# Optimization experiments

Hardware: AMD Instinct MI355X
Metric: run time of the kernel (lower is better)

Reference implementation:

```python
import jax, jax.numpy as jnp
import numpy as np

N_LAYER = 2
N_HEAD = 12
D = 768
B = 4
L = 1024
LN_EPS = 1e-6
NEG = jnp.float32(-1e9)


def setup_inputs() -> dict:
    key = jax.random.key(0)
    ks = jax.random.split(key, 12)
    s = 0.02
    wshp = (N_LAYER, 4, D, D)
    return {
        "h_a": jax.random.normal(ks[0], (B, L, D), jnp.float32),
        "h_b": jax.random.normal(ks[1], (B, L, D), jnp.float32),
        "adj_a": jax.random.randint(ks[2], (B, L, L), 0, 2, jnp.int32),
        "adj_b": jax.random.randint(ks[3], (B, L, L), 0, 2, jnp.int32),
        "adj_ab": jax.random.randint(ks[4], (B, L, L), 0, 2, jnp.int32),
        "adj_ba": jax.random.randint(ks[5], (B, L, L), 0, 2, jnp.int32),
        "Wq": jax.random.normal(ks[6], wshp, jnp.float32) * s,
        "Wk": jax.random.normal(ks[7], wshp, jnp.float32) * s,
        "Wv": jax.random.normal(ks[8], wshp, jnp.float32) * s,
        "Wf": jax.random.normal(ks[9], wshp, jnp.float32) * s,
        "ln_g": jnp.ones((N_LAYER, 4, D), jnp.float32),
        "ln_b": jnp.zeros((N_LAYER, 4, D), jnp.float32),
    }


def _mha(xq, xk, xv, mask, Wq, Wk, Wv, Wf, g, b):
    # xq: [B, Lq, D]; mask: [B, Lq, Lk] (0 = masked out)
    Bq, Lq, d = xq.shape
    dk = d // N_HEAD
    q = (xq @ Wq).reshape(Bq, Lq, N_HEAD, dk).transpose(0, 2, 1, 3)
    k = (xk @ Wk).reshape(Bq, -1, N_HEAD, dk).transpose(0, 2, 1, 3)
    v = (xv @ Wv).reshape(Bq, -1, N_HEAD, dk).transpose(0, 2, 1, 3)
    attn = jnp.einsum('bhqd,bhkd->bhqk', q, k) / jnp.sqrt(jnp.float32(dk))
    attn = jnp.where(mask[:, None, :, :] == 0, NEG, attn)
    attn = jax.nn.softmax(attn, axis=-1)
    o = jnp.einsum('bhqk,bhkd->bhqd', attn, v)
    o = o.transpose(0, 2, 1, 3).reshape(Bq, Lq, d)
    o = o @ Wf + xq  # residual (dropout is identity in eval)
    mu = jnp.mean(o, axis=-1, keepdims=True)
    var = jnp.var(o, axis=-1, keepdims=True)
    return (o - mu) * jax.lax.rsqrt(var + LN_EPS) * g + b


def reference(h_a, h_b, adj_a, adj_b, adj_ab, adj_ba, Wq, Wk, Wv, Wf, ln_g, ln_b):
    input_a, input_b = h_a, h_b
    for i in range(N_LAYER):
        a2a = _mha(h_a, h_a, h_a, adj_a, Wq[i, 0], Wk[i, 0], Wv[i, 0], Wf[i, 0], ln_g[i, 0], ln_b[i, 0])
        b2b = _mha(h_b, h_b, h_b, adj_b, Wq[i, 1], Wk[i, 1], Wv[i, 1], Wf[i, 1], ln_g[i, 1], ln_b[i, 1])
        a2b = _mha(h_b, h_a, h_a, adj_ab, Wq[i, 2], Wk[i, 2], Wv[i, 2], Wf[i, 2], ln_g[i, 2], ln_b[i, 2])
        b2a = _mha(h_a, h_b, h_b, adj_ba, Wq[i, 3], Wk[i, 3], Wv[i, 3], Wf[i, 3], ln_g[i, 3], ln_b[i, 3])
        h_a = jax.nn.relu(a2a + b2a)
        h_b = jax.nn.relu(b2b + a2b)
    return (input_a + h_a, input_b + h_b)
```

## Files before the change

### kernel.cpp

```cpp
#include <hip/hip_runtime.h>
#include <stdint.h>

#define NLAYER 2
#define NHEAD 12
#define D 768
#define BB 4
#define LL 1024
#define M (BB*LL)
#define DK 64

typedef unsigned short u16;
typedef unsigned int u32;
typedef unsigned long long u64;
typedef __attribute__((ext_vector_type(8))) __bf16 bf16x8;
typedef __attribute__((ext_vector_type(4))) float f32x4;

__device__ __forceinline__ u16 f2b(float f) {
  u32 u = __float_as_uint(f);
  u += 0x7fffu + ((u >> 16) & 1u);
  return (u16)(u >> 16);
}
__device__ __forceinline__ float b2f(u16 h) {
  return __uint_as_float(((u32)h) << 16);
}
__device__ __forceinline__ f32x4 mfma16(bf16x8 a, bf16x8 b, f32x4 c) {
  return __builtin_amdgcn_mfma_f32_16x16x32_bf16(a, b, c, 0, 0, 0);
}
__device__ __forceinline__ void gl_lds16(const u16* g, u16* l) {
  __builtin_amdgcn_global_load_lds((const __attribute__((address_space(1))) void*)(g),
                                   (__attribute__((address_space(3))) void*)(l), 16, 0, 0);
}

__global__ void cast_f32_bf16(const float* __restrict__ src, u16* __restrict__ dst, int n) {
  int i = (blockIdx.x * 256 + threadIdx.x) * 4;
  if (i + 3 < n) {
    float4 v = *(const float4*)(src + i);
    dst[i+0] = f2b(v.x); dst[i+1] = f2b(v.y); dst[i+2] = f2b(v.z); dst[i+3] = f2b(v.w);
  }
}

__global__ void wtrans(const float* __restrict__ Wq, const float* __restrict__ Wk,
                       const float* __restrict__ Wv, const float* __restrict__ Wf,
                       u16* __restrict__ wtr) {
  int z = blockIdx.z;
  int layer = z >> 4, mat = (z >> 2) & 3, s = z & 3;
  const float* src = (mat==0?Wq:mat==1?Wk:mat==2?Wv:Wf) + (size_t)(layer*4 + s)*D*D;
  u16* dst = wtr + (size_t)z*D*D;
  __shared__ float tile[32][33];
  int x0 = blockIdx.x*32, y0 = blockIdx.y*32;
  int tx = threadIdx.x & 31, ty = threadIdx.x >> 5;
  #pragma unroll
  for (int i=0;i<4;++i) tile[ty + i*8][tx] = src[(size_t)(y0 + ty + i*8)*D + x0 + tx];
  __syncthreads();
  #pragma unroll
  for (int i=0;i<4;++i) dst[(size_t)(x0 + ty + i*8)*D + y0 + tx] = f2b(tile[tx][ty + i*8]);
}

__global__ __launch_bounds__(256) void pack_adj(const int* __restrict__ a0, const int* __restrict__ a1,
                                                const int* __restrict__ a2, const int* __restrict__ a3,
                                                u64* __restrict__ mb) {
  const int s = blockIdx.y;
  const int* __restrict__ src = s==0?a0:s==1?a1:s==2?a2:a3;
  u64* dst = mb + (size_t)s * (BB*LL*LL/64);
  const int lane = threadIdx.x & 63;
  const int w0 = blockIdx.x*4 + (threadIdx.x>>6);
  const int wstep = gridDim.x*4;
  for (int w = w0; w < BB*LL*LL/64; w += wstep) {
    int v = src[(size_t)w*64 + lane];
    u64 m = __ballot(v != 0);
    if (lane == 0) dst[w] = m;
  }
}

__device__ __forceinline__ void gemm128(const u16* __restrict__ A, const u16* __restrict__ W,
                                        u16* __restrict__ C, int vtrans,
                                        int m0, int n0) {
  __shared__ __align__(16) u16 As[2][128*32];
  __shared__ __align__(16) u16 Bs[2][128*32];
  const int t = threadIdx.x;
  const int wave = t >> 6, lane = t & 63, lg = lane >> 4, lr = lane & 15;
  const int wr = wave >> 1, wc = wave & 1;
  f32x4 acc[4][4] = {};
  const int srow = wave*32 + (lane >> 2);
  const int scol = (lane & 3) << 3;
  const u16* ga0 = A + (size_t)(m0 + srow)*D + scol;
  const u16* gb0 = W + (size_t)(n0 + srow)*D + scol;
  const int l0 = (wave*32)*32, l1 = (wave*32 + 16)*32;

  for (int kk = 0; kk < D; kk += 64) {
    __syncthreads();
    #pragma unroll
    for (int hh=0; hh<2; ++hh) {
      const int ko = kk + hh*32;
      gl_lds16(ga0 + ko,        &As[hh][l0]);
      gl_lds16(ga0 + ko + 16*D, &As[hh][l1]);
      gl_lds16(gb0 + ko,        &Bs[hh][l0]);
      gl_lds16(gb0 + ko + 16*D, &Bs[hh][l1]);
    }
    __syncthreads();
    #pragma unroll
    for (int hh=0; hh<2; ++hh) {
      bf16x8 af[4], bfr[4];
      #pragma unroll
      for (int mi=0;mi<4;++mi) af[mi] = *(const bf16x8*)(&As[hh][(wr*64 + mi*16 + lr)*32 + lg*8]);
      #pragma unroll
      for (int ni=0;ni<4;++ni) bfr[ni] = *(const bf16x8*)(&Bs[hh][(wc*64 + ni*16 + lr)*32 + lg*8]);
      #pragma unroll
      for (int mi=0;mi<4;++mi)
        #pragma unroll
        for (int ni=0;ni<4;++ni)
          acc[mi][ni] = mfma16(af[mi], bfr[ni], acc[mi][ni]);
    }
  }

  if (!vtrans) {
    #pragma unroll
    for (int mi=0;mi<4;++mi)
      #pragma unroll
      for (int ni=0;ni<4;++ni) {
        int col = n0 + wc*64 + ni*16 + lr;
        #pragma unroll
        for (int r=0;r<4;++r) {
          int row = m0 + wr*64 + mi*16 + lg*4 + r;
          C[(size_t)row*D + col] = f2b(acc[mi][ni][r]);
        }
      }
  } else {
    #pragma unroll
    for (int mi=0;mi<4;++mi)
      #pragma unroll
      for (int ni=0;ni<4;++ni) {
        int col = n0 + wc*64 + ni*16 + lr;
        int h = col >> 6, d = col & 63;
        #pragma unroll
        for (int r=0;r<4;++r) {
          int row = m0 + wr*64 + mi*16 + lg*4 + r;
          int p = ((r >> 1) << 5) | (lg << 3) | (mi << 1) | (r & 1);
          int lperm = (row & ~63) | p;
          int b = row >> 10, l = lperm & 1023;
          C[(((size_t)((b*NHEAD + h)<<6) + d) << 10) + l] = f2b(acc[mi][ni][r]);
        }
      }
  }
}

__global__ __launch_bounds__(256) void qkv_gemm(const u16* __restrict__ hA, const u16* __restrict__ hB,
                        const u16* __restrict__ wtr,
                        u16* __restrict__ Qb, u16* __restrict__ Kb, u16* __restrict__ Vtb, int layer) {
  int bid = blockIdx.x + 32*(blockIdx.y + 6*blockIdx.z);
  int logical = (bid & 7)*288 + (bid >> 3);
  int z = logical / 192, rem = logical % 192;
  int x = rem / 6, y = rem % 6;
  int s = z / 3, which = z % 3;
  const u16* X;
  if (which == 0) X = (s==0||s==3) ? hA : hB;
  else            X = (s==0||s==2) ? hA : hB;
  const u16* W = wtr + (size_t)((layer*4 + which)*4 + s)*D*D;
  u16* Cb = (which==0 ? Qb : which==1 ? Kb : Vtb) + (size_t)s*M*D;
  gemm128(X, W, Cb, which == 2 ? 1 : 0, x*128, y*128);
}

__global__ __launch_bounds__(256) void oproj_gemm(const u16* __restrict__ Ob, const u16* __restrict__ wtr,
                          u16* __restrict__ OPb, int layer) {
  int bid = blockIdx.x + 32*(blockIdx.y + 6*blockIdx.z);
  int logical = (bid & 7)*96 + (bid >> 3);
  int s = logical / 192, rem = logical % 192;
  int x = rem / 6, y = rem % 6;
  const u16* W = wtr + (size_t)((layer*4 + 3)*4 + s)*D*D;
  gemm128(Ob + (size_t)s*M*D, W, OPb + (size_t)s*M*D, 0, x*128, y*128);
}

#define CSC 0.1803368801111204f

__global__ __launch_bounds__(512) void attn_kernel(const u16* __restrict__ Qb, const u16* __restrict__ Kb,
                           const u16* __restrict__ Vtb,
                           const u64* __restrict__ mbits,
                           u16* __restrict__ Ob) {
  int bid = blockIdx.x + 8*(blockIdx.y + 48*blockIdx.z);
  int logical = (bid & 7)*192 + (bid >> 3);
  const int qt = logical & 7;
  const int bhs = logical >> 3;
  const int s = bhs / 48;
  const int bh = bhs % 48;
  const int b = bh / NHEAD, h = bh % NHEAD;

  const int t = threadIdx.x, wave = t >> 6, lane = t & 63, lg = lane >> 4, lr = lane & 15;
  const u16* Q = Qb + (size_t)s*M*D;
  const u16* K = Kb + (size_t)s*M*D;
  u16* O = Ob + (size_t)s*M*D;
  const u64* mbs = mbits + (size_t)s*(BB*LL*LL/64) + (size_t)b*(LL*LL/64);

  __shared__ __align__(16) u16 Ks[64][72];
  __shared__ __align__(16) u16 Vts[64][72];

  const int q0 = qt*128 + wave*16;
  bf16x8 qf0 = *(const bf16x8*)(Q + (size_t)(b*LL + q0 + lr)*D + h*DK + lg*8);
  bf16x8 qf1 = *(const bf16x8*)(Q + (size_t)(b*LL + q0 + lr)*D + h*DK + 32 + lg*8);

  f32x4 of[4] = {};
  float lrow = 0.f;

  const int kr = t >> 3, kc = (t & 7) << 3;
  const u16* Kp  = K + (size_t)(b*LL + kr)*D + h*DK + kc;
  const u16* Vtp = Vtb + (size_t)s*M*D + ((size_t)(bh*64 + kr) << 10) + kc;

  uint4 ka = *(const uint4*)(Kp);
  uint4 va = *(const uint4*)(Vtp);
  const int mstride = LL/64;
  u64 mw = mbs[(size_t)(q0 + lr)*mstride];
  u64 mwn;

  for (int kt = 0; kt < LL; kt += 64) {
    __syncthreads();
    *(uint4*)(&Ks[kr][kc])  = ka;
    *(uint4*)(&Vts[kr][kc]) = va;
    if (kt + 64 < LL) {
      ka = *(const uint4*)(Kp + (size_t)(kt+64)*D);
      va = *(const uint4*)(Vtp + kt + 64);
      mwn = mbs[(size_t)(q0 + lr)*mstride + (kt >> 6) + 1];
    }
    __syncthreads();

    f32x4 sfr[4];
    __builtin_amdgcn_s_setprio(1);
    #pragma unroll
    for (int c=0;c<4;++c) {
      bf16x8 kf0 = *(const bf16x8*)(&Ks[c*16+lr][lg*8]);
      bf16x8 kf1 = *(const bf16x8*)(&Ks[c*16+lr][32 + lg*8]);
      f32x4 z = {0.f,0.f,0.f,0.f};
      z = mfma16(kf0, qf0, z);
      z = mfma16(kf1, qf1, z);
      sfr[c] = z;
    }
    __builtin_amdgcn_s_setprio(0);

    u32 wlo = (u32)(mw >> (lg*4));
    u32 whi = (u32)(mw >> (lg*4 + 32));
    float pw[4][4];
    #pragma unroll
    for (int c=0;c<4;++c) {
      u32 wsel = (c < 2) ? wlo : whi;
      int sh = (c & 1) << 4;
      #pragma unroll
      for (int r=0;r<4;++r) {
        float e = __builtin_amdgcn_exp2f(sfr[c][r]*CSC);
        e = ((wsel >> (sh + r)) & 1u) ? e : 0.f;
        pw[c][r] = e;
        lrow += e;
      }
    }
    mw = mwn;

    union { u32 u[4]; bf16x8 v; } a0, a1;
    #pragma unroll
    for (int c=0;c<4;++c) {
      a0.u[c] = (__float_as_uint(pw[c][0]) >> 16) | (__float_as_uint(pw[c][1]) & 0xffff0000u);
      a1.u[c] = (__float_as_uint(pw[c][2]) >> 16) | (__float_as_uint(pw[c][3]) & 0xffff0000u);
    }

    __builtin_amdgcn_s_setprio(1);
    #pragma unroll
    for (int ni=0;ni<4;++ni) {
      bf16x8 vf0 = *(const bf16x8*)(&Vts[ni*16+lr][lg*8]);
      bf16x8 vf1 = *(const bf16x8*)(&Vts[ni*16+lr][32 + lg*8]);
      of[ni] = mfma16(a0.v, vf0, of[ni]);
      of[ni] = mfma16(a1.v, vf1, of[ni]);
    }
    __builtin_amdgcn_s_setprio(0);
  }

  lrow += __shfl_xor(lrow, 16, 64);
  lrow += __shfl_xor(lrow, 32, 64);

  #pragma unroll
  for (int r=0;r<4;++r) {
    float l = __shfl(lrow, lg*4 + r, 64);
    float inv = 1.0f / fmaxf(l, 1e-35f);
    int row = b*LL + q0 + lg*4 + r;
    #pragma unroll
    for (int ni=0;ni<4;++ni)
      O[(size_t)row*D + h*DK + ni*16 + lr] = f2b(of[ni][r] * inv);
  }
}

__global__ __launch_bounds__(256) void epilogue(const u16* __restrict__ OPb,
                        u16* __restrict__ hA, u16* __restrict__ hB,
                        const float* __restrict__ lng, const float* __restrict__ lnb,
                        const float* __restrict__ inA, const float* __restrict__ inB,
                        float* __restrict__ outA, float* __restrict__ outB,
                        int layer, int last) {
  const int row = blockIdx.x;
  const int t = threadIdx.x;
  __shared__ float red[8];
  float lnv[4][3];
  #pragma unroll
  for (int s=0;s<4;++s) {
    const u16* xq = (s==0||s==3) ? hA : hB;
    float o[3]; float sum=0.f, sq=0.f;
    #pragma unroll
    for (int j=0;j<3;++j) {
      int c = t + j*256;
      float v = b2f(OPb[((size_t)s*M + row)*D + c]) + b2f(xq[(size_t)row*D + c]);
      o[j]=v; sum+=v; sq += v*v;
    }
    #pragma unroll
    for (int off=32; off>0; off>>=1) { sum += __shfl_down(sum, off, 64); sq += __shfl_down(sq, off, 64); }
    int wv = t>>6, ln = t&63;
    if (ln==0) { red[wv] = sum; red[4+wv] = sq; }
    __syncthreads();
    sum = red[0]+red[1]+red[2]+red[3];
    sq  = red[4]+red[5]+red[6]+red[7];
    __syncthreads();
    float mu = sum * (1.0f/D);
    float var = sq * (1.0f/D) - mu*mu;
    float rstd = rsqrtf(var + 1e-6f);
    #pragma unroll
    for (int j=0;j<3;++j) {
      int c = t + j*256;
      lnv[s][j] = (o[j]-mu)*rstd * lng[(layer*4+s)*D + c] + lnb[(layer*4+s)*D + c];
    }
  }
  #pragma unroll
  for (int j=0;j<3;++j) {
    int c = t + j*256;
    float ha = fmaxf(lnv[0][j]+lnv[3][j], 0.f);
    float hb = fmaxf(lnv[1][j]+lnv[2][j], 0.f);
    hA[(size_t)row*D + c] = f2b(ha);
    hB[(size_t)row*D + c] = f2b(hb);
    if (last) {
      outA[(size_t)row*D + c] = inA[(size_t)row*D + c] + ha;
      outB[(size_t)row*D + c] = inB[(size_t)row*D + c] + hb;
    }
  }
}

extern "C" void kernel_launch(void* const* d_in, const int* in_sizes, int n_in,
                              void* d_out, int out_size, void* d_ws, size_t ws_size,
                              hipStream_t stream) {
  const float* h_a = (const float*)d_in[0];
  const float* h_b = (const float*)d_in[1];
  const int* adjA  = (const int*)d_in[2];
  const int* adjB  = (const int*)d_in[3];
  const int* adjAB = (const int*)d_in[4];
  const int* adjBA = (const int*)d_in[5];
  const float* Wq  = (const float*)d_in[6];
  const float* Wk  = (const float*)d_in[7];
  const float* Wv  = (const float*)d_in[8];
  const float* Wf  = (const float*)d_in[9];
  const float* lng = (const float*)d_in[10];
  const float* lnb = (const float*)d_in[11];
  float* outA = (float*)d_out;
  float* outB = outA + (size_t)M*D;

  char* ws = (char*)d_ws;
  size_t off = 0;
  auto alloc = [&](size_t bytes) { void* p = ws + off; off += (bytes + 255) & ~(size_t)255; return p; };
  u16* wtr = (u16*)alloc((size_t)32*D*D*2);
  u16* hAb = (u16*)alloc((size_t)M*D*2);
  u16* hBb = (u16*)alloc((size_t)M*D*2);
  u16* Qb  = (u16*)alloc((size_t)4*M*D*2);
  u16* Kb  = (u16*)alloc((size_t)4*M*D*2);
  u16* Vtb = (u16*)alloc((size_t)4*M*D*2);
  u16* Ob  = (u16*)alloc((size_t)4*M*D*2);
  u64* mbits = (u64*)alloc((size_t)4*BB*LL*LL/64*8);
  u16* OPb = Qb;

  int n = M*D;
  cast_f32_bf16<<<dim3(n/4/256), 256, 0, stream>>>(h_a, hAb, n);
  cast_f32_bf16<<<dim3(n/4/256), 256, 0, stream>>>(h_b, hBb, n);
  wtrans<<<dim3(24,24,32), 256, 0, stream>>>(Wq, Wk, Wv, Wf, wtr);
  pack_adj<<<dim3(2048,4), 256, 0, stream>>>(adjA, adjB, adjAB, adjBA, mbits);

  for (int layer = 0; layer < NLAYER; ++layer) {
    qkv_gemm<<<dim3(32,6,12), 256, 0, stream>>>(hAb, hBb, wtr, Qb, Kb, Vtb, layer);
    attn_kernel<<<dim3(8,48,4), 512, 0, stream>>>(Qb, Kb, Vtb, mbits, Ob);
    oproj_gemm<<<dim3(32,6,4), 256, 0, stream>>>(Ob, wtr, OPb, layer);
    epilogue<<<dim3(M), 256, 0, stream>>>(OPb, hAb, hBb, lng, lnb, h_a, h_b, outA, outB,
                                          layer, layer == NLAYER-1 ? 1 : 0);
  }
}
```

Before: 482.8 us.

## Use 8 waves per GEMM tile and batch layernorm reductions in epilogue

```diff
diff --git a/kernel.cpp b/kernel.cpp
--- a/kernel.cpp
+++ b/kernel.cpp
@@ -79,36 +79,34 @@
   __shared__ __align__(16) u16 Bs[2][128*32];
   const int t = threadIdx.x;
   const int wave = t >> 6, lane = t & 63, lg = lane >> 4, lr = lane & 15;
-  const int wr = wave >> 1, wc = wave & 1;
-  f32x4 acc[4][4] = {};
-  const int srow = wave*32 + (lane >> 2);
+  const int wr = wave >> 2, wc = wave & 3;
+  f32x4 acc[4][2] = {};
+  const int srow = wave*16 + (lane >> 2);
   const int scol = (lane & 3) << 3;
   const u16* ga0 = A + (size_t)(m0 + srow)*D + scol;
   const u16* gb0 = W + (size_t)(n0 + srow)*D + scol;
-  const int l0 = (wave*32)*32, l1 = (wave*32 + 16)*32;
+  const int l0 = (wave*16)*32;
 
   for (int kk = 0; kk < D; kk += 64) {
     __syncthreads();
     #pragma unroll
     for (int hh=0; hh<2; ++hh) {
       const int ko = kk + hh*32;
-      gl_lds16(ga0 + ko,        &As[hh][l0]);
-      gl_lds16(ga0 + ko + 16*D, &As[hh][l1]);
-      gl_lds16(gb0 + ko,        &Bs[hh][l0]);
-      gl_lds16(gb0 + ko + 16*D, &Bs[hh][l1]);
+      gl_lds16(ga0 + ko, &As[hh][l0]);
+      gl_lds16(gb0 + ko, &Bs[hh][l0]);
     }
     __syncthreads();
     #pragma unroll
     for (int hh=0; hh<2; ++hh) {
-      bf16x8 af[4], bfr[4];
+      bf16x8 af[4], bfr[2];
       #pragma unroll
       for (int mi=0;mi<4;++mi) af[mi] = *(const bf16x8*)(&As[hh][(wr*64 + mi*16 + lr)*32 + lg*8]);
       #pragma unroll
-      for (int ni=0;ni<4;++ni) bfr[ni] = *(const bf16x8*)(&Bs[hh][(wc*64 + ni*16 + lr)*32 + lg*8]);
+      for (int ni=0;ni<2;++ni) bfr[ni] = *(const bf16x8*)(&Bs[hh][(wc*32 + ni*16 + lr)*32 + lg*8]);
       #pragma unroll
       for (int mi=0;mi<4;++mi)
         #pragma unroll
-        for (int ni=0;ni<4;++ni)
+        for (int ni=0;ni<2;++ni)
           acc[mi][ni] = mfma16(af[mi], bfr[ni], acc[mi][ni]);
     }
   }
@@ -117,8 +115,8 @@
     #pragma unroll
     for (int mi=0;mi<4;++mi)
       #pragma unroll
-      for (int ni=0;ni<4;++ni) {
-        int col = n0 + wc*64 + ni*16 + lr;
+      for (int ni=0;ni<2;++ni) {
+        int col = n0 + wc*32 + ni*16 + lr;
         #pragma unroll
         for (int r=0;r<4;++r) {
           int row = m0 + wr*64 + mi*16 + lg*4 + r;
@@ -129,8 +127,8 @@
     #pragma unroll
     for (int mi=0;mi<4;++mi)
       #pragma unroll
-      for (int ni=0;ni<4;++ni) {
-        int col = n0 + wc*64 + ni*16 + lr;
+      for (int ni=0;ni<2;++ni) {
+        int col = n0 + wc*32 + ni*16 + lr;
         int h = col >> 6, d = col & 63;
         #pragma unroll
         for (int r=0;r<4;++r) {
@@ -144,7 +142,7 @@
   }
 }
 
-__global__ __launch_bounds__(256) void qkv_gemm(const u16* __restrict__ hA, const u16* __restrict__ hB,
+__global__ __launch_bounds__(512) void qkv_gemm(const u16* __restrict__ hA, const u16* __restrict__ hB,
                         const u16* __restrict__ wtr,
                         u16* __restrict__ Qb, u16* __restrict__ Kb, u16* __restrict__ Vtb, int layer) {
   int bid = blockIdx.x + 32*(blockIdx.y + 6*blockIdx.z);
@@ -160,7 +158,7 @@
   gemm128(X, W, Cb, which == 2 ? 1 : 0, x*128, y*128);
 }
 
-__global__ __launch_bounds__(256) void oproj_gemm(const u16* __restrict__ Ob, const u16* __restrict__ wtr,
+__global__ __launch_bounds__(512) void oproj_gemm(const u16* __restrict__ Ob, const u16* __restrict__ wtr,
                           u16* __restrict__ OPb, int layer) {
   int bid = blockIdx.x + 32*(blockIdx.y + 6*blockIdx.z);
   int logical = (bid & 7)*96 + (bid >> 3);
@@ -291,33 +289,46 @@
                         int layer, int last) {
   const int row = blockIdx.x;
   const int t = threadIdx.x;
-  __shared__ float red[8];
-  float lnv[4][3];
+  __shared__ float red[4][8];
+  float av[3], bv[3];
+  #pragma unroll
+  for (int j=0;j<3;++j) {
+    int c = t + j*256;
+    av[j] = b2f(hA[(size_t)row*D + c]);
+    bv[j] = b2f(hB[(size_t)row*D + c]);
+  }
+  float o[4][3]; float sum[4] = {0,0,0,0}, sq[4] = {0,0,0,0};
   #pragma unroll
   for (int s=0;s<4;++s) {
-    const u16* xq = (s==0||s==3) ? hA : hB;
-    float o[3]; float sum=0.f, sq=0.f;
     #pragma unroll
     for (int j=0;j<3;++j) {
       int c = t + j*256;
-      float v = b2f(OPb[((size_t)s*M + row)*D + c]) + b2f(xq[(size_t)row*D + c]);
-      o[j]=v; sum+=v; sq += v*v;
-    }
-    #pragma unroll
-    for (int off=32; off>0; off>>=1) { sum += __shfl_down(sum, off, 64); sq += __shfl_down(sq, off, 64); }
-    int wv = t>>6, ln = t&63;
-    if (ln==0) { red[wv] = sum; red[4+wv] = sq; }
-    __syncthreads();
-    sum = red[0]+red[1]+red[2]+red[3];
-    sq  = red[4]+red[5]+red[6]+red[7];
-    __syncthreads();
-    float mu = sum * (1.0f/D);
-    float var = sq * (1.0f/D) - mu*mu;
+      float v = b2f(OPb[((size_t)s*M + row)*D + c]) + ((s==0||s==3) ? av[j] : bv[j]);
+      o[s][j]=v; sum[s]+=v; sq[s]+=v*v;
+    }
+  }
+  #pragma unroll
+  for (int off=32; off>0; off>>=1)
+    #pragma unroll
+    for (int s=0;s<4;++s) { sum[s] += __shfl_down(sum[s], off, 64); sq[s] += __shfl_down(sq[s], off, 64); }
+  int wv = t>>6, ln = t&63;
+  if (ln==0) {
+    #pragma unroll
+    for (int s=0;s<4;++s) { red[wv][s] = sum[s]; red[wv][4+s] = sq[s]; }
+  }
+  __syncthreads();
+  float lnv[4][3];
+  #pragma unroll
+  for (int s=0;s<4;++s) {
+    float sm = red[0][s]+red[1][s]+red[2][s]+red[3][s];
+    float sk = red[0][4+s]+red[1][4+s]+red[2][4+s]+red[3][4+s];
+    float mu = sm * (1.0f/D);
+    float var = sk * (1.0f/D) - mu*mu;
     float rstd = rsqrtf(var + 1e-6f);
     #pragma unroll
     for (int j=0;j<3;++j) {
       int c = t + j*256;
-      lnv[s][j] = (o[j]-mu)*rstd * lng[(layer*4+s)*D + c] + lnb[(layer*4+s)*D + c];
+      lnv[s][j] = (o[s][j]-mu)*rstd * lng[(layer*4+s)*D + c] + lnb[(layer*4+s)*D + c];
     }
   }
   #pragma unroll
@@ -372,9 +383,9 @@
   pack_adj<<<dim3(2048,4), 256, 0, stream>>>(adjA, adjB, adjAB, adjBA, mbits);
 
   for (int layer = 0; layer < NLAYER; ++layer) {
-    qkv_gemm<<<dim3(32,6,12), 256, 0, stream>>>(hAb, hBb, wtr, Qb, Kb, Vtb, layer);
+    qkv_gemm<<<dim3(32,6,12), 512, 0, stream>>>(hAb, hBb, wtr, Qb, Kb, Vtb, layer);
     attn_kernel<<<dim3(8,48,4), 512, 0, stream>>>(Qb, Kb, Vtb, mbits, Ob);
-    oproj_gemm<<<dim3(32,6,4), 256, 0, stream>>>(Ob, wtr, OPb, layer);
+    oproj_gemm<<<dim3(32,6,4), 512, 0, stream>>>(Ob, wtr, OPb, layer);
     epilogue<<<dim3(M), 256, 0, stream>>>(OPb, hAb, hBb, lng, lnb, h_a, h_b, outA, outB,
                                           layer, layer == NLAYER-1 ? 1 : 0);
   }
```

Result: faster. 437.4 us (-9.4%).
